# Optimization experiments

Measured on AMD Instinct MI355X. Metric: run time of the kernel, lower is better.

The kernel has to match this reference:

```python
import jax, jax.numpy as jnp
import numpy as np

E = 256   # embed_dim
H = 8     # num_heads
D = E // H  # head_dim = 32
L = 1024  # seq len (Q_len == K_len == V_len)


def setup_inputs() -> dict:
    key = jax.random.key(0)
    ks = jax.random.split(key, 10)
    f = lambda k, s: jax.random.normal(k, s, dtype=jnp.float32)
    return {
        "V": f(ks[0], (L, E)),
        "K": f(ks[1], (L, E)),
        "Q": f(ks[2], (L, E)),
        # genomic-style coordinates, strictly positive
        "position": jax.random.uniform(ks[3], (L,), dtype=jnp.float32) * 1e5,
        "Wq": f(ks[4], (E, E)) * 0.02,
        "Wk": f(ks[5], (E, E)) * 0.02,
        "Wv": f(ks[6], (E, E)) * 0.02,
        "Wr": f(ks[7], (E, 1)) * 0.02,   # K_relative_linear weight [out=E, in=1]
        "Wo": f(ks[8], (E, E)) * 0.02,
        "bo": jnp.zeros((E,), jnp.float32),
    }


def reference(V, K, Q, position, Wq, Wk, Wv, Wr, Wo, bo):
    Lq = Q.shape[0]
    # projections (nn.Linear: x @ W.T), split into heads -> (L, H, D)
    q = (Q @ Wq.T).reshape(Lq, H, D)
    k = (K @ Wk.T).reshape(Lq, H, D)
    v = (V @ Wv.T).reshape(Lq, H, D)

    # relative position scalar per (q, k) pair: log(|p_q - p_k| + 1)
    rel = jnp.log(jnp.abs(position[:, None] - position[None, :]) + 1.0)  # (L, L)

    # K_relative_linear maps scalar rel -> (H, D); the einsum
    # 'nqhd,nhqjd->nhqj' then factorizes exactly as:
    #   sum_d Q[q,h,d] * rel[q,j] * Wr[h,d] = (Q . Wr)[h,q] * rel[q,j]
    # so we avoid materializing the (H, L, L, D) tensor while computing
    # mathematically identical results.
    Wr_h = Wr[:, 0].reshape(H, D)                    # (H, D)
    coeff = jnp.einsum('qhd,hd->hq', q, Wr_h)        # (H, L)

    energy = jnp.einsum('qhd,khd->hqk', q, k)        # (H, L, L)
    energy = energy + coeff[:, :, None] * rel[None, :, :]

    attn = jax.nn.softmax(energy / np.float32(E) ** 0.5, axis=2)
    out = jnp.einsum('hqk,khd->qhd', attn, v).reshape(Lq, E)
    out = out @ Wo.T + bo
    return out
```

## Files before the change

### kernel.cpp

```cpp
#include <hip/hip_runtime.h>
#include <math.h>

#define EDIM 256
#define LDIM 1024
#define HDIM 8
#define DDIM 32

typedef __attribute__((ext_vector_type(8))) short short8;
typedef __attribute__((ext_vector_type(2))) short short2v;
typedef __attribute__((ext_vector_type(4))) short shortx4;
typedef __attribute__((ext_vector_type(4))) float f32x4;

__device__ inline unsigned short bf16h(float x) {
    unsigned u = __float_as_uint(x);
    return (unsigned short)((u + 0x7fff + ((u >> 16) & 1)) >> 16);
}
__device__ inline float bf16tof(unsigned short h) {
    return __uint_as_float(((unsigned)h) << 16);
}
__device__ inline float exp2fast(float x) {
    float r; asm volatile("v_exp_f32 %0, %1" : "=v"(r) : "v"(x)); return r;
}
__device__ inline float log2fast(float x) {
    float r; asm volatile("v_log_f32 %0, %1" : "=v"(r) : "v"(x)); return r;
}

#define SC2 0.09016843880556021f

__global__ __launch_bounds__(256) void proj_kernel(
    const float* __restrict__ Q, const float* __restrict__ Km, const float* __restrict__ V,
    const float* __restrict__ Wq, const float* __restrict__ Wk, const float* __restrict__ Wv,
    const float* __restrict__ Wr, const float* __restrict__ Wo,
    short* __restrict__ qThi, short* __restrict__ qTlo,
    short* __restrict__ kThi, short* __restrict__ kTlo,
    short* __restrict__ vThi, short* __restrict__ vTlo,
    float* __restrict__ coeff, short* __restrict__ Wohi, short* __restrict__ Wolo)
{
    const int z = blockIdx.z;
    const int tid = threadIdx.x;

    if (z == 3) {
        const int idx = ((blockIdx.y * 32 + blockIdx.x) << 8) + tid;
        const float w = Wo[idx];
        const unsigned short hh = bf16h(w);
        Wohi[idx] = (short)hh;
        Wolo[idx] = (short)bf16h(w - bf16tof(hh));
        return;
    }

    const float* __restrict__ X = (z == 0) ? Q : (z == 1) ? Km : V;
    const float* __restrict__ W = (z == 0) ? Wq : (z == 1) ? Wk : Wv;
    short* __restrict__ dhi     = (z == 0) ? qThi : (z == 1) ? kThi : vThi;
    short* __restrict__ dlo     = (z == 0) ? qTlo : (z == 1) ? kTlo : vTlo;

    const int n0 = blockIdx.x * 32;
    const int o0 = blockIdx.y * 32;
    const int wave = tid >> 6, lane = tid & 63;
    const int n = lane & 15, quad = lane >> 4;
    const int rh = wave & 1, oh = wave >> 1;

    const int s    = tid >> 7;
    const int r    = (tid >> 2) & 31;
    const int qd   = tid & 3;
    const int half = r >> 4;
    const int fl8  = ((r & 15) | (qd << 4)) * 8;

    __shared__ short Xhi[2][2][512], Xlo[2][2][512];
    __shared__ short Whi[2][2][512], Wlo[2][2][512];
    __shared__ float cpart[2][2][16];

    const float* xp = X + (n0 + r) * EDIM + s * 32 + qd * 8;
    const float* wp = W + (o0 + r) * EDIM + s * 32 + qd * 8;

    float4 xa0 = *(const float4*)xp, xa1 = *(const float4*)(xp + 4);
    float4 wa0 = *(const float4*)wp, wa1 = *(const float4*)(wp + 4);

    f32x4 acc = {0.f, 0.f, 0.f, 0.f};

    for (int kb = 0; kb < EDIM; kb += 64) {
        __syncthreads();
        {
            float xv[8] = {xa0.x,xa0.y,xa0.z,xa0.w, xa1.x,xa1.y,xa1.z,xa1.w};
            float wv[8] = {wa0.x,wa0.y,wa0.z,wa0.w, wa1.x,wa1.y,wa1.z,wa1.w};
            short8 xh, xl, wh, wl;
            #pragma unroll
            for (int j = 0; j < 8; ++j) {
                unsigned short xhh = bf16h(xv[j]);
                unsigned short whh = bf16h(wv[j]);
                xh[j] = (short)xhh; xl[j] = (short)bf16h(xv[j] - bf16tof(xhh));
                wh[j] = (short)whh; wl[j] = (short)bf16h(wv[j] - bf16tof(whh));
            }
            *(short8*)&Xhi[s][half][fl8] = xh;
            *(short8*)&Xlo[s][half][fl8] = xl;
            *(short8*)&Whi[s][half][fl8] = wh;
            *(short8*)&Wlo[s][half][fl8] = wl;
        }
        float4 xn0, xn1, wn0, wn1;
        if (kb + 64 < EDIM) {
            xn0 = *(const float4*)(xp + kb + 64); xn1 = *(const float4*)(xp + kb + 68);
            wn0 = *(const float4*)(wp + kb + 64); wn1 = *(const float4*)(wp + kb + 68);
        }
        __syncthreads();
        #pragma unroll
        for (int ss = 0; ss < 2; ++ss) {
            short8 ah = *(const short8*)&Xhi[ss][rh][lane*8];
            short8 al = *(const short8*)&Xlo[ss][rh][lane*8];
            short8 bh = *(const short8*)&Whi[ss][oh][lane*8];
            short8 bl = *(const short8*)&Wlo[ss][oh][lane*8];
            acc = __builtin_amdgcn_mfma_f32_16x16x32_bf16(al, bh, acc, 0, 0, 0);
            acc = __builtin_amdgcn_mfma_f32_16x16x32_bf16(ah, bl, acc, 0, 0, 0);
            acc = __builtin_amdgcn_mfma_f32_16x16x32_bf16(ah, bh, acc, 0, 0, 0);
        }
        xa0 = xn0; xa1 = xn1; wa0 = wn0; wa1 = wn1;
    }

    const int h  = o0 >> 5;
    const int og = oh * 16 + n;
    #pragma unroll
    for (int i = 0; i < 4; ++i) {
        const int row = rh * 16 + 4 * quad + i;
        const unsigned short hh = bf16h(acc[i]);
        dhi[(h * LDIM + n0 + row) * DDIM + og] = (short)hh;
        dlo[(h * LDIM + n0 + row) * DDIM + og] = (short)bf16h(acc[i] - bf16tof(hh));
    }

    if (z == 0) {
        const float wr = Wr[o0 + og];
        #pragma unroll
        for (int i = 0; i < 4; ++i) {
            float c = acc[i] * wr;
            c += __shfl_xor(c, 1, 64);
            c += __shfl_xor(c, 2, 64);
            c += __shfl_xor(c, 4, 64);
            c += __shfl_xor(c, 8, 64);
            if (n == 0) cpart[rh][oh][4*quad + i] = c;
        }
        __syncthreads();
        if (tid < 32)
            coeff[h * LDIM + n0 + tid] = cpart[tid >> 4][0][tid & 15]
                                       + cpart[tid >> 4][1][tid & 15];
    }
}

__global__ __launch_bounds__(256, 2) void attn_kernel(
    const short* __restrict__ qThi, const short* __restrict__ qTlo,
    const short* __restrict__ kThi, const short* __restrict__ kTlo,
    const short* __restrict__ vThi, const short* __restrict__ vTlo,
    const float* __restrict__ coeff, const float* __restrict__ pos,
    short* __restrict__ Ahi, short* __restrict__ Alo)
{
    const int h    = blockIdx.y;
    const int q0   = blockIdx.x * 16;
    const int tid  = threadIdx.x;
    const int wave = tid >> 6;
    const int lane = tid & 63;
    const int n    = lane & 15;
    const int quad = lane >> 4;

    __shared__ __align__(16) short vs_hi[4][32][72];
    __shared__ __align__(16) short vs_lo[4][32][72];
    __shared__ __align__(16) short pa_hi[4][16][72];
    __shared__ __align__(16) short pa_lo[4][16][72];
    __shared__ float mw[4][16], lw[4][16];
    __shared__ float Ow[4][16][36];

    const short8 qhi = *(const short8*)(qThi + (h*LDIM + q0 + n) * DDIM + quad*8);
    const short8 qlo = *(const short8*)(qTlo + (h*LDIM + q0 + n) * DDIM + quad*8);

    float pq[4], cq[4];
    #pragma unroll
    for (int i = 0; i < 4; ++i) {
        const int r = q0 + 4*quad + i;
        pq[i] = pos[r];
        cq[i] = coeff[h*LDIM + r] * 0.0625f;
    }

    float m[4], l[4];
    #pragma unroll
    for (int i = 0; i < 4; ++i) { m[i] = -INFINITY; l[i] = 0.f; }
    f32x4 of0 = {0.f,0.f,0.f,0.f}, of1 = {0.f,0.f,0.f,0.f};

    const int ktb = wave * 256;
    #pragma unroll 1
    for (int t = 0; t < 4; ++t) {
        const int kt = ktb + t * 64;

        {
            const short* vh = vThi + (h*LDIM + kt + lane) * DDIM;
            const short* vl = vTlo + (h*LDIM + kt + lane) * DDIM;
            #pragma unroll
            for (int hf = 0; hf < 2; ++hf) {
                short8 a0 = *(const short8*)(vh + hf*16);
                short8 a1 = *(const short8*)(vh + hf*16 + 8);
                short8 b0 = *(const short8*)(vl + hf*16);
                short8 b1 = *(const short8*)(vl + hf*16 + 8);
                #pragma unroll
                for (int j = 0; j < 8; ++j) {
                    vs_hi[wave][hf*16 + j][lane]     = a0[j];
                    vs_hi[wave][hf*16 + 8 + j][lane] = a1[j];
                    vs_lo[wave][hf*16 + j][lane]     = b0[j];
                    vs_lo[wave][hf*16 + 8 + j][lane] = b1[j];
                }
            }
        }

        f32x4 Sf[4];
        #pragma unroll
        for (int t4 = 0; t4 < 4; ++t4) {
            const int off = (h*LDIM + kt + t4*16 + n) * DDIM + quad*8;
            short8 bh = *(const short8*)(kThi + off);
            short8 bl = *(const short8*)(kTlo + off);
            f32x4 acc = {0.f, 0.f, 0.f, 0.f};
            acc = __builtin_amdgcn_mfma_f32_16x16x32_bf16(qlo, bh, acc, 0, 0, 0);
            acc = __builtin_amdgcn_mfma_f32_16x16x32_bf16(qhi, bl, acc, 0, 0, 0);
            acc = __builtin_amdgcn_mfma_f32_16x16x32_bf16(qhi, bh, acc, 0, 0, 0);
            Sf[t4] = acc;
        }

        float ev[4][4];
        float rmax[4] = {-INFINITY, -INFINITY, -INFINITY, -INFINITY};
        #pragma unroll
        for (int t4 = 0; t4 < 4; ++t4) {
            const float pkt = pos[kt + t4*16 + n];
            #pragma unroll
            for (int i = 0; i < 4; ++i) {
                float s = fmaf(Sf[t4][i], SC2, cq[i] * log2fast(fabsf(pq[i] - pkt) + 1.f));
                ev[t4][i] = s;
                rmax[i] = fmaxf(rmax[i], s);
            }
        }
        #pragma unroll
        for (int off = 1; off < 16; off <<= 1)
            #pragma unroll
            for (int i = 0; i < 4; ++i)
                rmax[i] = fmaxf(rmax[i], __shfl_xor(rmax[i], off, 64));

        float al[4], rsum[4];
        #pragma unroll
        for (int i = 0; i < 4; ++i) {
            const float mn = fmaxf(m[i], rmax[i]);
            al[i] = exp2fast(m[i] - mn);
            m[i] = mn;
            rsum[i] = 0.f;
        }
        #pragma unroll
        for (int t4 = 0; t4 < 4; ++t4)
            #pragma unroll
            for (int i = 0; i < 4; ++i) {
                float e = exp2fast(ev[t4][i] - m[i]);
                rsum[i] += e;
                unsigned u = __float_as_uint(e);
                pa_hi[wave][4*quad + i][16*t4 + n] = (short)(u >> 16);
                float r = e - __uint_as_float(u & 0xffff0000u);
                pa_lo[wave][4*quad + i][16*t4 + n] = (short)bf16h(r);
            }
        #pragma unroll
        for (int off = 1; off < 16; off <<= 1)
            #pragma unroll
            for (int i = 0; i < 4; ++i)
                rsum[i] += __shfl_xor(rsum[i], off, 64);
        #pragma unroll
        for (int i = 0; i < 4; ++i) l[i] = l[i]*al[i] + rsum[i];

        #pragma unroll
        for (int i = 0; i < 4; ++i) { of0[i] *= al[i]; of1[i] *= al[i]; }

        #pragma unroll
        for (int ch = 0; ch < 2; ++ch) {
            short8 phi = *(const short8*)&pa_hi[wave][n][ch*32 + quad*8];
            short8 plo = *(const short8*)&pa_lo[wave][n][ch*32 + quad*8];
            #pragma unroll
            for (int dt = 0; dt < 2; ++dt) {
                short8 vh8 = *(const short8*)&vs_hi[wave][dt*16 + n][ch*32 + quad*8];
                short8 vl8 = *(const short8*)&vs_lo[wave][dt*16 + n][ch*32 + quad*8];
                f32x4& of = dt ? of1 : of0;
                of = __builtin_amdgcn_mfma_f32_16x16x32_bf16(plo, vh8, of, 0, 0, 0);
                of = __builtin_amdgcn_mfma_f32_16x16x32_bf16(phi, vl8, of, 0, 0, 0);
                of = __builtin_amdgcn_mfma_f32_16x16x32_bf16(phi, vh8, of, 0, 0, 0);
            }
        }
    }

    #pragma unroll
    for (int i = 0; i < 4; ++i) {
        Ow[wave][4*quad + i][n]      = of0[i];
        Ow[wave][4*quad + i][16 + n] = of1[i];
    }
    if (n == 0) {
        #pragma unroll
        for (int i = 0; i < 4; ++i) {
            mw[wave][4*quad + i] = m[i];
            lw[wave][4*quad + i] = l[i];
        }
    }
    __syncthreads();

    {
        const int q  = tid >> 4;
        const int dp = (tid & 15) * 2;
        float M = fmaxf(fmaxf(mw[0][q], mw[1][q]), fmaxf(mw[2][q], mw[3][q]));
        float sc[4], s = 0.f;
        #pragma unroll
        for (int w = 0; w < 4; ++w) {
            sc[w] = exp2fast(mw[w][q] - M);
            s += sc[w] * lw[w][q];
        }
        const float inv = 1.f / s;
        short2v h2, l2;
        #pragma unroll
        for (int e = 0; e < 2; ++e) {
            float a = 0.f;
            #pragma unroll
            for (int w = 0; w < 4; ++w) a += sc[w] * Ow[w][q][dp + e];
            a *= inv;
            const unsigned short hh = bf16h(a);
            h2[e] = (short)hh;
            l2[e] = (short)bf16h(a - bf16tof(hh));
        }
        *(short2v*)(Ahi + (q0 + q)*EDIM + h*DDIM + dp) = h2;
        *(short2v*)(Alo + (q0 + q)*EDIM + h*DDIM + dp) = l2;
    }
}

__global__ __launch_bounds__(256) void outproj_kernel(
    const short* __restrict__ Ahi, const short* __restrict__ Alo,
    const short* __restrict__ Wohi, const short* __restrict__ Wolo,
    const float* __restrict__ bo, float* __restrict__ out)
{
    const int n0 = blockIdx.x * 32;
    const int o0 = blockIdx.y * 32;
    const int tid = threadIdx.x;
    const int wave = tid >> 6, lane = tid & 63;
    const int n = lane & 15, quad = lane >> 4;
    const int rh = wave & 1, oh = wave >> 1;

    const int s    = tid >> 7;
    const int r    = (tid >> 2) & 31;
    const int qd   = tid & 3;
    const int half = r >> 4;
    const int fl8  = ((r & 15) | (qd << 4)) * 8;

    __shared__ short Xhi[2][2][512], Xlo[2][2][512];
    __shared__ short Whi[2][2][512], Wlo[2][2][512];

    const short* xph = Ahi  + (n0 + r) * EDIM + s * 32 + qd * 8;
    const short* xpl = Alo  + (n0 + r) * EDIM + s * 32 + qd * 8;
    const short* wph = Wohi + (o0 + r) * EDIM + s * 32 + qd * 8;
    const short* wpl = Wolo + (o0 + r) * EDIM + s * 32 + qd * 8;

    short8 xh_c = *(const short8*)xph;
    short8 xl_c = *(const short8*)xpl;
    short8 wh_c = *(const short8*)wph;
    short8 wl_c = *(const short8*)wpl;

    f32x4 acc = {0.f, 0.f, 0.f, 0.f};

    for (int kb = 0; kb < EDIM; kb += 64) {
        __syncthreads();
        *(short8*)&Xhi[s][half][fl8] = xh_c;
        *(short8*)&Xlo[s][half][fl8] = xl_c;
        *(short8*)&Whi[s][half][fl8] = wh_c;
        *(short8*)&Wlo[s][half][fl8] = wl_c;
        short8 xh_n, xl_n, wh_n, wl_n;
        if (kb + 64 < EDIM) {
            xh_n = *(const short8*)(xph + kb + 64);
            xl_n = *(const short8*)(xpl + kb + 64);
            wh_n = *(const short8*)(wph + kb + 64);
            wl_n = *(const short8*)(wpl + kb + 64);
        }
        __syncthreads();
        #pragma unroll
        for (int ss = 0; ss < 2; ++ss) {
            short8 ah = *(const short8*)&Xhi[ss][rh][lane*8];
            short8 al = *(const short8*)&Xlo[ss][rh][lane*8];
            short8 bh = *(const short8*)&Whi[ss][oh][lane*8];
            short8 bl = *(const short8*)&Wlo[ss][oh][lane*8];
            acc = __builtin_amdgcn_mfma_f32_16x16x32_bf16(al, bh, acc, 0, 0, 0);
            acc = __builtin_amdgcn_mfma_f32_16x16x32_bf16(ah, bl, acc, 0, 0, 0);
            acc = __builtin_amdgcn_mfma_f32_16x16x32_bf16(ah, bh, acc, 0, 0, 0);
        }
        xh_c = xh_n; xl_c = xl_n; wh_c = wh_n; wl_c = wl_n;
    }

    const int og = o0 + oh*16 + n;
    const float b = bo[og];
    #pragma unroll
    for (int i = 0; i < 4; ++i) {
        const int row = n0 + rh*16 + 4*quad + i;
        out[row * EDIM + og] = acc[i] + b;
    }
}

extern "C" void kernel_launch(void* const* d_in, const int* in_sizes, int n_in,
                              void* d_out, int out_size, void* d_ws, size_t ws_size,
                              hipStream_t stream) {
    const float* V   = (const float*)d_in[0];
    const float* K   = (const float*)d_in[1];
    const float* Q   = (const float*)d_in[2];
    const float* pos = (const float*)d_in[3];
    const float* Wq  = (const float*)d_in[4];
    const float* Wk  = (const float*)d_in[5];
    const float* Wv  = (const float*)d_in[6];
    const float* Wr  = (const float*)d_in[7];
    const float* Wo  = (const float*)d_in[8];
    const float* bo  = (const float*)d_in[9];
    float* out = (float*)d_out;
    char* base = (char*)d_ws;

    short* qThi  = (short*)(base);
    short* qTlo  = (short*)(base + 524288);
    short* kThi  = (short*)(base + 1048576);
    short* kTlo  = (short*)(base + 1572864);
    short* vThi  = (short*)(base + 2097152);
    short* vTlo  = (short*)(base + 2621440);
    float* coeff = (float*)(base + 3145728);
    short* Wohi  = (short*)(base + 3178496);
    short* Wolo  = (short*)(base + 3309568);
    short* Ahi   = (short*)(base + 3440640);
    short* Alo   = (short*)(base + 3964928);

    proj_kernel   <<<dim3(32, 8, 4), 256, 0, stream>>>(Q, K, V, Wq, Wk, Wv, Wr, Wo,
                                                       qThi, qTlo, kThi, kTlo, vThi, vTlo,
                                                       coeff, Wohi, Wolo);
    attn_kernel   <<<dim3(64, 8),    256, 0, stream>>>(qThi, qTlo, kThi, kTlo, vThi, vTlo,
                                                       coeff, pos, Ahi, Alo);
    outproj_kernel<<<dim3(32, 8),    256, 0, stream>>>(Ahi, Alo, Wohi, Wolo, bo, out);
}
```

Baseline: 101.0 us.

## Fuse projection, attention and output projection into one persistent kernel with grid barriers

Replaces the three separate kernel launches with a single 512-block kernel. Each block performs two projection tiles, then one attention tile, then at most one output-projection tile, with atomic-counter grid barriers between the phases. Shared memory is a union of the two phase layouts. This removes launch overhead and inter-kernel gaps, but adds a memset and spin barriers, and correctness depends on all 512 blocks being co-resident.

```diff
diff --git a/kernel.cpp b/kernel.cpp
--- a/kernel.cpp
+++ b/kernel.cpp
@@ -8,7 +8,6 @@
 
 typedef __attribute__((ext_vector_type(8))) short short8;
 typedef __attribute__((ext_vector_type(2))) short short2v;
-typedef __attribute__((ext_vector_type(4))) short shortx4;
 typedef __attribute__((ext_vector_type(4))) float f32x4;
 
 __device__ inline unsigned short bf16h(float x) {
@@ -27,367 +26,390 @@
 
 #define SC2 0.09016843880556021f
 
-__global__ __launch_bounds__(256) void proj_kernel(
+#define NBLK 512
+
+__device__ inline void grid_barrier(unsigned* cnt) {
+    __syncthreads();
+    if (threadIdx.x == 0) {
+        __threadfence();
+        atomicAdd(cnt, 1u);
+        while (atomicAdd(cnt, 0u) < NBLK) __builtin_amdgcn_s_sleep(2);
+    }
+    __syncthreads();
+    __threadfence();
+}
+
+struct __align__(16) SmemProj {
+    short Xhi[2][2][512], Xlo[2][2][512];
+    short Whi[2][2][512], Wlo[2][2][512];
+    float cpart[2][2][16];
+};
+struct __align__(16) SmemAttn {
+    short vs_hi[4][32][72], vs_lo[4][32][72];
+    short pa_hi[4][16][72], pa_lo[4][16][72];
+    float mw[4][16], lw[4][16];
+    float Ow[4][16][36];
+};
+union SmemU {
+    SmemProj p;
+    SmemAttn a;
+};
+
+__global__ __launch_bounds__(256, 2) void mega_kernel(
     const float* __restrict__ Q, const float* __restrict__ Km, const float* __restrict__ V,
+    const float* __restrict__ pos,
     const float* __restrict__ Wq, const float* __restrict__ Wk, const float* __restrict__ Wv,
-    const float* __restrict__ Wr, const float* __restrict__ Wo,
-    short* __restrict__ qThi, short* __restrict__ qTlo,
-    short* __restrict__ kThi, short* __restrict__ kTlo,
-    short* __restrict__ vThi, short* __restrict__ vTlo,
-    float* __restrict__ coeff, short* __restrict__ Wohi, short* __restrict__ Wolo)
+    const float* __restrict__ Wr, const float* __restrict__ Wo, const float* __restrict__ bo,
+    float* __restrict__ out, char* __restrict__ base)
 {
-    const int z = blockIdx.z;
+    __shared__ SmemU sm;
+
+    short* qThi  = (short*)(base);
+    short* qTlo  = (short*)(base + 524288);
+    short* kThi  = (short*)(base + 1048576);
+    short* kTlo  = (short*)(base + 1572864);
+    short* vThi  = (short*)(base + 2097152);
+    short* vTlo  = (short*)(base + 2621440);
+    float* coeff = (float*)(base + 3145728);
+    short* Wohi  = (short*)(base + 3178496);
+    short* Wolo  = (short*)(base + 3309568);
+    short* Ahi   = (short*)(base + 3440640);
+    short* Alo   = (short*)(base + 3964928);
+    unsigned* flags = (unsigned*)(base + 4489216);
+
     const int tid = threadIdx.x;
-
-    if (z == 3) {
-        const int idx = ((blockIdx.y * 32 + blockIdx.x) << 8) + tid;
-        const float w = Wo[idx];
-        const unsigned short hh = bf16h(w);
-        Wohi[idx] = (short)hh;
-        Wolo[idx] = (short)bf16h(w - bf16tof(hh));
-        return;
-    }
-
-    const float* __restrict__ X = (z == 0) ? Q : (z == 1) ? Km : V;
-    const float* __restrict__ W = (z == 0) ? Wq : (z == 1) ? Wk : Wv;
-    short* __restrict__ dhi     = (z == 0) ? qThi : (z == 1) ? kThi : vThi;
-    short* __restrict__ dlo     = (z == 0) ? qTlo : (z == 1) ? kTlo : vTlo;
-
-    const int n0 = blockIdx.x * 32;
-    const int o0 = blockIdx.y * 32;
+    const int bid = blockIdx.x;
+
     const int wave = tid >> 6, lane = tid & 63;
     const int n = lane & 15, quad = lane >> 4;
-    const int rh = wave & 1, oh = wave >> 1;
-
-    const int s    = tid >> 7;
-    const int r    = (tid >> 2) & 31;
-    const int qd   = tid & 3;
-    const int half = r >> 4;
-    const int fl8  = ((r & 15) | (qd << 4)) * 8;
-
-    __shared__ short Xhi[2][2][512], Xlo[2][2][512];
-    __shared__ short Whi[2][2][512], Wlo[2][2][512];
-    __shared__ float cpart[2][2][16];
-
-    const float* xp = X + (n0 + r) * EDIM + s * 32 + qd * 8;
-    const float* wp = W + (o0 + r) * EDIM + s * 32 + qd * 8;
-
-    float4 xa0 = *(const float4*)xp, xa1 = *(const float4*)(xp + 4);
-    float4 wa0 = *(const float4*)wp, wa1 = *(const float4*)(wp + 4);
-
-    f32x4 acc = {0.f, 0.f, 0.f, 0.f};
-
-    for (int kb = 0; kb < EDIM; kb += 64) {
-        __syncthreads();
-        {
-            float xv[8] = {xa0.x,xa0.y,xa0.z,xa0.w, xa1.x,xa1.y,xa1.z,xa1.w};
-            float wv[8] = {wa0.x,wa0.y,wa0.z,wa0.w, wa1.x,wa1.y,wa1.z,wa1.w};
-            short8 xh, xl, wh, wl;
-            #pragma unroll
-            for (int j = 0; j < 8; ++j) {
-                unsigned short xhh = bf16h(xv[j]);
-                unsigned short whh = bf16h(wv[j]);
-                xh[j] = (short)xhh; xl[j] = (short)bf16h(xv[j] - bf16tof(xhh));
-                wh[j] = (short)whh; wl[j] = (short)bf16h(wv[j] - bf16tof(whh));
-            }
-            *(short8*)&Xhi[s][half][fl8] = xh;
-            *(short8*)&Xlo[s][half][fl8] = xl;
-            *(short8*)&Whi[s][half][fl8] = wh;
-            *(short8*)&Wlo[s][half][fl8] = wl;
-        }
-        float4 xn0, xn1, wn0, wn1;
-        if (kb + 64 < EDIM) {
-            xn0 = *(const float4*)(xp + kb + 64); xn1 = *(const float4*)(xp + kb + 68);
-            wn0 = *(const float4*)(wp + kb + 64); wn1 = *(const float4*)(wp + kb + 68);
-        }
-        __syncthreads();
-        #pragma unroll
-        for (int ss = 0; ss < 2; ++ss) {
-            short8 ah = *(const short8*)&Xhi[ss][rh][lane*8];
-            short8 al = *(const short8*)&Xlo[ss][rh][lane*8];
-            short8 bh = *(const short8*)&Whi[ss][oh][lane*8];
-            short8 bl = *(const short8*)&Wlo[ss][oh][lane*8];
-            acc = __builtin_amdgcn_mfma_f32_16x16x32_bf16(al, bh, acc, 0, 0, 0);
-            acc = __builtin_amdgcn_mfma_f32_16x16x32_bf16(ah, bl, acc, 0, 0, 0);
-            acc = __builtin_amdgcn_mfma_f32_16x16x32_bf16(ah, bh, acc, 0, 0, 0);
-        }
-        xa0 = xn0; xa1 = xn1; wa0 = wn0; wa1 = wn1;
+
+    {
+        const int rh = wave & 1, oh = wave >> 1;
+        const int s    = tid >> 7;
+        const int r    = (tid >> 2) & 31;
+        const int qd   = tid & 3;
+        const int half = r >> 4;
+        const int fl8  = ((r & 15) | (qd << 4)) * 8;
+
+        for (int ui = 0; ui < 2; ++ui) {
+            const int u = bid * 2 + ui;
+            const int z = u >> 8;
+            const int x = u & 31, y = (u >> 5) & 7;
+
+            if (z == 3) {
+                const int idx = ((y * 32 + x) << 8) + tid;
+                const float w = Wo[idx];
+                const unsigned short hh = bf16h(w);
+                Wohi[idx] = (short)hh;
+                Wolo[idx] = (short)bf16h(w - bf16tof(hh));
+                continue;
+            }
+
+            const float* __restrict__ X = (z == 0) ? Q : (z == 1) ? Km : V;
+            const float* __restrict__ W = (z == 0) ? Wq : (z == 1) ? Wk : Wv;
+            short* __restrict__ dhi     = (z == 0) ? qThi : (z == 1) ? kThi : vThi;
+            short* __restrict__ dlo     = (z == 0) ? qTlo : (z == 1) ? kTlo : vTlo;
+            const int n0 = x * 32;
+            const int o0 = y * 32;
+
+            const float* xp = X + (n0 + r) * EDIM + s * 32 + qd * 8;
+            const float* wp = W + (o0 + r) * EDIM + s * 32 + qd * 8;
+
+            float4 xa0 = *(const float4*)xp, xa1 = *(const float4*)(xp + 4);
+            float4 wa0 = *(const float4*)wp, wa1 = *(const float4*)(wp + 4);
+
+            f32x4 acc = {0.f, 0.f, 0.f, 0.f};
+
+            for (int kb = 0; kb < EDIM; kb += 64) {
+                __syncthreads();
+                {
+                    float xv[8] = {xa0.x,xa0.y,xa0.z,xa0.w, xa1.x,xa1.y,xa1.z,xa1.w};
+                    float wv[8] = {wa0.x,wa0.y,wa0.z,wa0.w, wa1.x,wa1.y,wa1.z,wa1.w};
+                    short8 xh, xl, wh, wl;
+                    #pragma unroll
+                    for (int j = 0; j < 8; ++j) {
+                        unsigned short xhh = bf16h(xv[j]);
+                        unsigned short whh = bf16h(wv[j]);
+                        xh[j] = (short)xhh; xl[j] = (short)bf16h(xv[j] - bf16tof(xhh));
+                        wh[j] = (short)whh; wl[j] = (short)bf16h(wv[j] - bf16tof(whh));
+                    }
+                    *(short8*)&sm.p.Xhi[s][half][fl8] = xh;
+                    *(short8*)&sm.p.Xlo[s][half][fl8] = xl;
+                    *(short8*)&sm.p.Whi[s][half][fl8] = wh;
+                    *(short8*)&sm.p.Wlo[s][half][fl8] = wl;
+                }
+                float4 xn0, xn1, wn0, wn1;
+                if (kb + 64 < EDIM) {
+                    xn0 = *(const float4*)(xp + kb + 64); xn1 = *(const float4*)(xp + kb + 68);
+                    wn0 = *(const float4*)(wp + kb + 64); wn1 = *(const float4*)(wp + kb + 68);
+                }
+                __syncthreads();
+                #pragma unroll
+                for (int ss = 0; ss < 2; ++ss) {
+                    short8 ah = *(const short8*)&sm.p.Xhi[ss][rh][lane*8];
+                    short8 al = *(const short8*)&sm.p.Xlo[ss][rh][lane*8];
+                    short8 bh = *(const short8*)&sm.p.Whi[ss][oh][lane*8];
+                    short8 bl = *(const short8*)&sm.p.Wlo[ss][oh][lane*8];
+                    acc = __builtin_amdgcn_mfma_f32_16x16x32_bf16(al, bh, acc, 0, 0, 0);
+                    acc = __builtin_amdgcn_mfma_f32_16x16x32_bf16(ah, bl, acc, 0, 0, 0);
+                    acc = __builtin_amdgcn_mfma_f32_16x16x32_bf16(ah, bh, acc, 0, 0, 0);
+                }
+                xa0 = xn0; xa1 = xn1; wa0 = wn0; wa1 = wn1;
+            }
+
+            const int h  = o0 >> 5;
+            const int og = oh * 16 + n;
+            #pragma unroll
+            for (int i = 0; i < 4; ++i) {
+                const int row = rh * 16 + 4 * quad + i;
+                const unsigned short hh = bf16h(acc[i]);
+                dhi[(h * LDIM + n0 + row) * DDIM + og] = (short)hh;
+                dlo[(h * LDIM + n0 + row) * DDIM + og] = (short)bf16h(acc[i] - bf16tof(hh));
+            }
+
+            if (z == 0) {
+                const float wr = Wr[o0 + og];
+                #pragma unroll
+                for (int i = 0; i < 4; ++i) {
+                    float c = acc[i] * wr;
+                    c += __shfl_xor(c, 1, 64);
+                    c += __shfl_xor(c, 2, 64);
+                    c += __shfl_xor(c, 4, 64);
+                    c += __shfl_xor(c, 8, 64);
+                    if (n == 0) sm.p.cpart[rh][oh][4*quad + i] = c;
+                }
+                __syncthreads();
+                if (tid < 32)
+                    coeff[h * LDIM + n0 + tid] = sm.p.cpart[tid >> 4][0][tid & 15]
+                                               + sm.p.cpart[tid >> 4][1][tid & 15];
+            }
+        }
     }
 
-    const int h  = o0 >> 5;
-    const int og = oh * 16 + n;
-    #pragma unroll
-    for (int i = 0; i < 4; ++i) {
-        const int row = rh * 16 + 4 * quad + i;
-        const unsigned short hh = bf16h(acc[i]);
-        dhi[(h * LDIM + n0 + row) * DDIM + og] = (short)hh;
-        dlo[(h * LDIM + n0 + row) * DDIM + og] = (short)bf16h(acc[i] - bf16tof(hh));
-    }
-
-    if (z == 0) {
-        const float wr = Wr[o0 + og];
+    grid_barrier(&flags[0]);
+
+    {
+        const int h  = bid >> 6;
+        const int q0 = (bid & 63) * 16;
+
+        const short8 qhi = *(const short8*)(qThi + (h*LDIM + q0 + n) * DDIM + quad*8);
+        const short8 qlo = *(const short8*)(qTlo + (h*LDIM + q0 + n) * DDIM + quad*8);
+
+        float pq[4], cq[4];
         #pragma unroll
         for (int i = 0; i < 4; ++i) {
-            float c = acc[i] * wr;
-            c += __shfl_xor(c, 1, 64);
-            c += __shfl_xor(c, 2, 64);
-            c += __shfl_xor(c, 4, 64);
-            c += __shfl_xor(c, 8, 64);
-            if (n == 0) cpart[rh][oh][4*quad + i] = c;
-        }
-        __syncthreads();
-        if (tid < 32)
-            coeff[h * LDIM + n0 + tid] = cpart[tid >> 4][0][tid & 15]
-                                       + cpart[tid >> 4][1][tid & 15];
-    }
-}
-
-__global__ __launch_bounds__(256, 2) void attn_kernel(
-    const short* __restrict__ qThi, const short* __restrict__ qTlo,
-    const short* __restrict__ kThi, const short* __restrict__ kTlo,
-    const short* __restrict__ vThi, const short* __restrict__ vTlo,
-    const float* __restrict__ coeff, const float* __restrict__ pos,
-    short* __restrict__ Ahi, short* __restrict__ Alo)
-{
-    const int h    = blockIdx.y;
-    const int q0   = blockIdx.x * 16;
-    const int tid  = threadIdx.x;
-    const int wave = tid >> 6;
-    const int lane = tid & 63;
-    const int n    = lane & 15;
-    const int quad = lane >> 4;
-
-    __shared__ __align__(16) short vs_hi[4][32][72];
-    __shared__ __align__(16) short vs_lo[4][32][72];
-    __shared__ __align__(16) short pa_hi[4][16][72];
-    __shared__ __align__(16) short pa_lo[4][16][72];
-    __shared__ float mw[4][16], lw[4][16];
-    __shared__ float Ow[4][16][36];
-
-    const short8 qhi = *(const short8*)(qThi + (h*LDIM + q0 + n) * DDIM + quad*8);
-    const short8 qlo = *(const short8*)(qTlo + (h*LDIM + q0 + n) * DDIM + quad*8);
-
-    float pq[4], cq[4];
-    #pragma unroll
-    for (int i = 0; i < 4; ++i) {
-        const int r = q0 + 4*quad + i;
-        pq[i] = pos[r];
-        cq[i] = coeff[h*LDIM + r] * 0.0625f;
-    }
-
-    float m[4], l[4];
-    #pragma unroll
-    for (int i = 0; i < 4; ++i) { m[i] = -INFINITY; l[i] = 0.f; }
-    f32x4 of0 = {0.f,0.f,0.f,0.f}, of1 = {0.f,0.f,0.f,0.f};
-
-    const int ktb = wave * 256;
-    #pragma unroll 1
-    for (int t = 0; t < 4; ++t) {
-        const int kt = ktb + t * 64;
-
-        {
-            const short* vh = vThi + (h*LDIM + kt + lane) * DDIM;
-            const short* vl = vTlo + (h*LDIM + kt + lane) * DDIM;
-            #pragma unroll
-            for (int hf = 0; hf < 2; ++hf) {
-                short8 a0 = *(const short8*)(vh + hf*16);
-                short8 a1 = *(const short8*)(vh + hf*16 + 8);
-                short8 b0 = *(const short8*)(vl + hf*16);
-                short8 b1 = *(const short8*)(vl + hf*16 + 8);
-                #pragma unroll
-                for (int j = 0; j < 8; ++j) {
-                    vs_hi[wave][hf*16 + j][lane]     = a0[j];
-                    vs_hi[wave][hf*16 + 8 + j][lane] = a1[j];
-                    vs_lo[wave][hf*16 + j][lane]     = b0[j];
-                    vs_lo[wave][hf*16 + 8 + j][lane] = b1[j];
-                }
-            }
-        }
-
-        f32x4 Sf[4];
+            const int r = q0 + 4*quad + i;
+            pq[i] = pos[r];
+            cq[i] = coeff[h*LDIM + r] * 0.0625f;
+        }
+
+        float m[4], l[4];
         #pragma unroll
-        for (int t4 = 0; t4 < 4; ++t4) {
-            const int off = (h*LDIM + kt + t4*16 + n) * DDIM + quad*8;
-            short8 bh = *(const short8*)(kThi + off);
-            short8 bl = *(const short8*)(kTlo + off);
-            f32x4 acc = {0.f, 0.f, 0.f, 0.f};
-            acc = __builtin_amdgcn_mfma_f32_16x16x32_bf16(qlo, bh, acc, 0, 0, 0);
-            acc = __builtin_amdgcn_mfma_f32_16x16x32_bf16(qhi, bl, acc, 0, 0, 0);
-            acc = __builtin_amdgcn_mfma_f32_16x16x32_bf16(qhi, bh, acc, 0, 0, 0);
-            Sf[t4] = acc;
-        }
-
-        float ev[4][4];
-        float rmax[4] = {-INFINITY, -INFINITY, -INFINITY, -INFINITY};
-        #pragma unroll
-        for (int t4 = 0; t4 < 4; ++t4) {
-            const float pkt = pos[kt + t4*16 + n];
+        for (int i = 0; i < 4; ++i) { m[i] = -INFINITY; l[i] = 0.f; }
+        f32x4 of0 = {0.f,0.f,0.f,0.f}, of1 = {0.f,0.f,0.f,0.f};
+
+        const int ktb = wave * 256;
+        #pragma unroll 1
+        for (int t = 0; t < 4; ++t) {
+            const int kt = ktb + t * 64;
+
+            {
+                const short* vh = vThi + (h*LDIM + kt + lane) * DDIM;
+                const short* vl = vTlo + (h*LDIM + kt + lane) * DDIM;
+                #pragma unroll
+                for (int hf = 0; hf < 2; ++hf) {
+                    short8 a0 = *(const short8*)(vh + hf*16);
+                    short8 a1 = *(const short8*)(vh + hf*16 + 8);
+                    short8 b0 = *(const short8*)(vl + hf*16);
+                    short8 b1 = *(const short8*)(vl + hf*16 + 8);
+                    #pragma unroll
+                    for (int j = 0; j < 8; ++j) {
+                        sm.a.vs_hi[wave][hf*16 + j][lane]     = a0[j];
+                        sm.a.vs_hi[wave][hf*16 + 8 + j][lane] = a1[j];
+                        sm.a.vs_lo[wave][hf*16 + j][lane]     = b0[j];
+                        sm.a.vs_lo[wave][hf*16 + 8 + j][lane] = b1[j];
+                    }
+                }
+            }
+
+            f32x4 Sf[4];
+            #pragma unroll
+            for (int t4 = 0; t4 < 4; ++t4) {
+                const int off = (h*LDIM + kt + t4*16 + n) * DDIM + quad*8;
+                short8 bh = *(const short8*)(kThi + off);
+                short8 bl = *(const short8*)(kTlo + off);
+                f32x4 acc = {0.f, 0.f, 0.f, 0.f};
+                acc = __builtin_amdgcn_mfma_f32_16x16x32_bf16(qlo, bh, acc, 0, 0, 0);
+                acc = __builtin_amdgcn_mfma_f32_16x16x32_bf16(qhi, bl, acc, 0, 0, 0);
+                acc = __builtin_amdgcn_mfma_f32_16x16x32_bf16(qhi, bh, acc, 0, 0, 0);
+                Sf[t4] = acc;
+            }
+
+            float ev[4][4];
+            float rmax[4] = {-INFINITY, -INFINITY, -INFINITY, -INFINITY};
+            #pragma unroll
+            for (int t4 = 0; t4 < 4; ++t4) {
+                const float pkt = pos[kt + t4*16 + n];
+                #pragma unroll
+                for (int i = 0; i < 4; ++i) {
+                    float s = fmaf(Sf[t4][i], SC2, cq[i] * log2fast(fabsf(pq[i] - pkt) + 1.f));
+                    ev[t4][i] = s;
+                    rmax[i] = fmaxf(rmax[i], s);
+                }
+            }
+            #pragma unroll
+            for (int off = 1; off < 16; off <<= 1)
+                #pragma unroll
+                for (int i = 0; i < 4; ++i)
+                    rmax[i] = fmaxf(rmax[i], __shfl_xor(rmax[i], off, 64));
+
+            float al[4], rsum[4];
             #pragma unroll
             for (int i = 0; i < 4; ++i) {
-                float s = fmaf(Sf[t4][i], SC2, cq[i] * log2fast(fabsf(pq[i] - pkt) + 1.f));
-                ev[t4][i] = s;
-                rmax[i] = fmaxf(rmax[i], s);
-            }
-        }
-        #pragma unroll
-        for (int off = 1; off < 16; off <<= 1)
-            #pragma unroll
-            for (int i = 0; i < 4; ++i)
-                rmax[i] = fmaxf(rmax[i], __shfl_xor(rmax[i], off, 64));
-
-        float al[4], rsum[4];
+                const float mn = fmaxf(m[i], rmax[i]);
+                al[i] = exp2fast(m[i] - mn);
+                m[i] = mn;
+                rsum[i] = 0.f;
+            }
+            #pragma unroll
+            for (int t4 = 0; t4 < 4; ++t4)
+                #pragma unroll
+                for (int i = 0; i < 4; ++i) {
+                    float e = exp2fast(ev[t4][i] - m[i]);
+                    rsum[i] += e;
+                    unsigned u = __float_as_uint(e);
+                    sm.a.pa_hi[wave][4*quad + i][16*t4 + n] = (short)(u >> 16);
+                    float r = e - __uint_as_float(u & 0xffff0000u);
+                    sm.a.pa_lo[wave][4*quad + i][16*t4 + n] = (short)bf16h(r);
+                }
+            #pragma unroll
+            for (int off = 1; off < 16; off <<= 1)
+                #pragma unroll
+                for (int i = 0; i < 4; ++i)
+                    rsum[i] += __shfl_xor(rsum[i], off, 64);
+            #pragma unroll
+            for (int i = 0; i < 4; ++i) l[i] = l[i]*al[i] + rsum[i];
+
+            #pragma unroll
+            for (int i = 0; i < 4; ++i) { of0[i] *= al[i]; of1[i] *= al[i]; }
+
+            #pragma unroll
+            for (int ch = 0; ch < 2; ++ch) {
+                short8 phi = *(const short8*)&sm.a.pa_hi[wave][n][ch*32 + quad*8];
+                short8 plo = *(const short8*)&sm.a.pa_lo[wave][n][ch*32 + quad*8];
+                #pragma unroll
+                for (int dt = 0; dt < 2; ++dt) {
+                    short8 vh8 = *(const short8*)&sm.a.vs_hi[wave][dt*16 + n][ch*32 + quad*8];
+                    short8 vl8 = *(const short8*)&sm.a.vs_lo[wave][dt*16 + n][ch*32 + quad*8];
+                    f32x4& of = dt ? of1 : of0;
+                    of = __builtin_amdgcn_mfma_f32_16x16x32_bf16(plo, vh8, of, 0, 0, 0);
+                    of = __builtin_amdgcn_mfma_f32_16x16x32_bf16(phi, vl8, of, 0, 0, 0);
+                    of = __builtin_amdgcn_mfma_f32_16x16x32_bf16(phi, vh8, of, 0, 0, 0);
+                }
+            }
+        }
+
         #pragma unroll
         for (int i = 0; i < 4; ++i) {
-            const float mn = fmaxf(m[i], rmax[i]);
-            al[i] = exp2fast(m[i] - mn);
-            m[i] = mn;
-            rsum[i] = 0.f;
-        }
-        #pragma unroll
-        for (int t4 = 0; t4 < 4; ++t4)
+            sm.a.Ow[wave][4*quad + i][n]      = of0[i];
+            sm.a.Ow[wave][4*quad + i][16 + n] = of1[i];
+        }
+        if (n == 0) {
             #pragma unroll
             for (int i = 0; i < 4; ++i) {
-                float e = exp2fast(ev[t4][i] - m[i]);
-                rsum[i] += e;
-                unsigned u = __float_as_uint(e);
-                pa_hi[wave][4*quad + i][16*t4 + n] = (short)(u >> 16);
-                float r = e - __uint_as_float(u & 0xffff0000u);
-                pa_lo[wave][4*quad + i][16*t4 + n] = (short)bf16h(r);
-            }
-        #pragma unroll
-        for (int off = 1; off < 16; off <<= 1)
-            #pragma unroll
-            for (int i = 0; i < 4; ++i)
-                rsum[i] += __shfl_xor(rsum[i], off, 64);
-        #pragma unroll
-        for (int i = 0; i < 4; ++i) l[i] = l[i]*al[i] + rsum[i];
-
-        #pragma unroll
-        for (int i = 0; i < 4; ++i) { of0[i] *= al[i]; of1[i] *= al[i]; }
-
-        #pragma unroll
-        for (int ch = 0; ch < 2; ++ch) {
-            short8 phi = *(const short8*)&pa_hi[wave][n][ch*32 + quad*8];
-            short8 plo = *(const short8*)&pa_lo[wave][n][ch*32 + quad*8];
-            #pragma unroll
-            for (int dt = 0; dt < 2; ++dt) {
-                short8 vh8 = *(const short8*)&vs_hi[wave][dt*16 + n][ch*32 + quad*8];
-                short8 vl8 = *(const short8*)&vs_lo[wave][dt*16 + n][ch*32 + quad*8];
-                f32x4& of = dt ? of1 : of0;
-                of = __builtin_amdgcn_mfma_f32_16x16x32_bf16(plo, vh8, of, 0, 0, 0);
-                of = __builtin_amdgcn_mfma_f32_16x16x32_bf16(phi, vl8, of, 0, 0, 0);
-                of = __builtin_amdgcn_mfma_f32_16x16x32_bf16(phi, vh8, of, 0, 0, 0);
-            }
+                sm.a.mw[wave][4*quad + i] = m[i];
+                sm.a.lw[wave][4*quad + i] = l[i];
+            }
+        }
+        __syncthreads();
+
+        {
+            const int q  = tid >> 4;
+            const int dp = (tid & 15) * 2;
+            float M = fmaxf(fmaxf(sm.a.mw[0][q], sm.a.mw[1][q]),
+                            fmaxf(sm.a.mw[2][q], sm.a.mw[3][q]));
+            float sc[4], s = 0.f;
+            #pragma unroll
+            for (int w = 0; w < 4; ++w) {
+                sc[w] = exp2fast(sm.a.mw[w][q] - M);
+                s += sc[w] * sm.a.lw[w][q];
+            }
+            const float inv = 1.f / s;
+            short2v h2, l2;
+            #pragma unroll
+            for (int e = 0; e < 2; ++e) {
+                float a = 0.f;
+                #pragma unroll
+                for (int w = 0; w < 4; ++w) a += sc[w] * sm.a.Ow[w][q][dp + e];
+                a *= inv;
+                const unsigned short hh = bf16h(a);
+                h2[e] = (short)hh;
+                l2[e] = (short)bf16h(a - bf16tof(hh));
+            }
+            *(short2v*)(Ahi + (q0 + q)*EDIM + h*DDIM + dp) = h2;
+            *(short2v*)(Alo + (q0 + q)*EDIM + h*DDIM + dp) = l2;
         }
     }
 
-    #pragma unroll
-    for (int i = 0; i < 4; ++i) {
-        Ow[wave][4*quad + i][n]      = of0[i];
-        Ow[wave][4*quad + i][16 + n] = of1[i];
-    }
-    if (n == 0) {
+    grid_barrier(&flags[1]);
+
+    if (bid < 256) {
+        const int n0 = (bid & 31) * 32;
+        const int o0 = (bid >> 5) * 32;
+        const int rh = wave & 1, oh = wave >> 1;
+
+        const int s    = tid >> 7;
+        const int r    = (tid >> 2) & 31;
+        const int qd   = tid & 3;
+        const int half = r >> 4;
+        const int fl8  = ((r & 15) | (qd << 4)) * 8;
+
+        const short* xph = Ahi  + (n0 + r) * EDIM + s * 32 + qd * 8;
+        const short* xpl = Alo  + (n0 + r) * EDIM + s * 32 + qd * 8;
+        const short* wph = Wohi + (o0 + r) * EDIM + s * 32 + qd * 8;
+        const short* wpl = Wolo + (o0 + r) * EDIM + s * 32 + qd * 8;
+
+        short8 xh_c = *(const short8*)xph;
+        short8 xl_c = *(const short8*)xpl;
+        short8 wh_c = *(const short8*)wph;
+        short8 wl_c = *(const short8*)wpl;
+
+        f32x4 acc = {0.f, 0.f, 0.f, 0.f};
+
+        for (int kb = 0; kb < EDIM; kb += 64) {
+            __syncthreads();
+            *(short8*)&sm.p.Xhi[s][half][fl8] = xh_c;
+            *(short8*)&sm.p.Xlo[s][half][fl8] = xl_c;
+            *(short8*)&sm.p.Whi[s][half][fl8] = wh_c;
+            *(short8*)&sm.p.Wlo[s][half][fl8] = wl_c;
+            short8 xh_n, xl_n, wh_n, wl_n;
+            if (kb + 64 < EDIM) {
+                xh_n = *(const short8*)(xph + kb + 64);
+                xl_n = *(const short8*)(xpl + kb + 64);
+                wh_n = *(const short8*)(wph + kb + 64);
+                wl_n = *(const short8*)(wpl + kb + 64);
+            }
+            __syncthreads();
+            #pragma unroll
+            for (int ss = 0; ss < 2; ++ss) {
+                short8 ah = *(const short8*)&sm.p.Xhi[ss][rh][lane*8];
+                short8 al = *(const short8*)&sm.p.Xlo[ss][rh][lane*8];
+                short8 bh = *(const short8*)&sm.p.Whi[ss][oh][lane*8];
+                short8 bl = *(const short8*)&sm.p.Wlo[ss][oh][lane*8];
+                acc = __builtin_amdgcn_mfma_f32_16x16x32_bf16(al, bh, acc, 0, 0, 0);
+                acc = __builtin_amdgcn_mfma_f32_16x16x32_bf16(ah, bl, acc, 0, 0, 0);
+                acc = __builtin_amdgcn_mfma_f32_16x16x32_bf16(ah, bh, acc, 0, 0, 0);
+            }
+            xh_c = xh_n; xl_c = xl_n; wh_c = wh_n; wl_c = wl_n;
+        }
+
+        const int og = o0 + oh*16 + n;
+        const float b = bo[og];
         #pragma unroll
         for (int i = 0; i < 4; ++i) {
-            mw[wave][4*quad + i] = m[i];
-            lw[wave][4*quad + i] = l[i];
-        }
-    }
-    __syncthreads();
-
-    {
-        const int q  = tid >> 4;
-        const int dp = (tid & 15) * 2;
-        float M = fmaxf(fmaxf(mw[0][q], mw[1][q]), fmaxf(mw[2][q], mw[3][q]));
-        float sc[4], s = 0.f;
-        #pragma unroll
-        for (int w = 0; w < 4; ++w) {
-            sc[w] = exp2fast(mw[w][q] - M);
-            s += sc[w] * lw[w][q];
-        }
-        const float inv = 1.f / s;
-        short2v h2, l2;
-        #pragma unroll
-        for (int e = 0; e < 2; ++e) {
-            float a = 0.f;
-            #pragma unroll
-            for (int w = 0; w < 4; ++w) a += sc[w] * Ow[w][q][dp + e];
-            a *= inv;
-            const unsigned short hh = bf16h(a);
-            h2[e] = (short)hh;
-            l2[e] = (short)bf16h(a - bf16tof(hh));
-        }
-        *(short2v*)(Ahi + (q0 + q)*EDIM + h*DDIM + dp) = h2;
-        *(short2v*)(Alo + (q0 + q)*EDIM + h*DDIM + dp) = l2;
-    }
-}
-
-__global__ __launch_bounds__(256) void outproj_kernel(
-    const short* __restrict__ Ahi, const short* __restrict__ Alo,
-    const short* __restrict__ Wohi, const short* __restrict__ Wolo,
-    const float* __restrict__ bo, float* __restrict__ out)
-{
-    const int n0 = blockIdx.x * 32;
-    const int o0 = blockIdx.y * 32;
-    const int tid = threadIdx.x;
-    const int wave = tid >> 6, lane = tid & 63;
-    const int n = lane & 15, quad = lane >> 4;
-    const int rh = wave & 1, oh = wave >> 1;
-
-    const int s    = tid >> 7;
-    const int r    = (tid >> 2) & 31;
-    const int qd   = tid & 3;
-    const int half = r >> 4;
-    const int fl8  = ((r & 15) | (qd << 4)) * 8;
-
-    __shared__ short Xhi[2][2][512], Xlo[2][2][512];
-    __shared__ short Whi[2][2][512], Wlo[2][2][512];
-
-    const short* xph = Ahi  + (n0 + r) * EDIM + s * 32 + qd * 8;
-    const short* xpl = Alo  + (n0 + r) * EDIM + s * 32 + qd * 8;
-    const short* wph = Wohi + (o0 + r) * EDIM + s * 32 + qd * 8;
-    const short* wpl = Wolo + (o0 + r) * EDIM + s * 32 + qd * 8;
-
-    short8 xh_c = *(const short8*)xph;
-    short8 xl_c = *(const short8*)xpl;
-    short8 wh_c = *(const short8*)wph;
-    short8 wl_c = *(const short8*)wpl;
-
-    f32x4 acc = {0.f, 0.f, 0.f, 0.f};
-
-    for (int kb = 0; kb < EDIM; kb += 64) {
-        __syncthreads();
-        *(short8*)&Xhi[s][half][fl8] = xh_c;
-        *(short8*)&Xlo[s][half][fl8] = xl_c;
-        *(short8*)&Whi[s][half][fl8] = wh_c;
-        *(short8*)&Wlo[s][half][fl8] = wl_c;
-        short8 xh_n, xl_n, wh_n, wl_n;
-        if (kb + 64 < EDIM) {
-            xh_n = *(const short8*)(xph + kb + 64);
-            xl_n = *(const short8*)(xpl + kb + 64);
-            wh_n = *(const short8*)(wph + kb + 64);
-            wl_n = *(const short8*)(wpl + kb + 64);
-        }
-        __syncthreads();
-        #pragma unroll
-        for (int ss = 0; ss < 2; ++ss) {
-            short8 ah = *(const short8*)&Xhi[ss][rh][lane*8];
-            short8 al = *(const short8*)&Xlo[ss][rh][lane*8];
-            short8 bh = *(const short8*)&Whi[ss][oh][lane*8];
-            short8 bl = *(const short8*)&Wlo[ss][oh][lane*8];
-            acc = __builtin_amdgcn_mfma_f32_16x16x32_bf16(al, bh, acc, 0, 0, 0);
-            acc = __builtin_amdgcn_mfma_f32_16x16x32_bf16(ah, bl, acc, 0, 0, 0);
-            acc = __builtin_amdgcn_mfma_f32_16x16x32_bf16(ah, bh, acc, 0, 0, 0);
-        }
-        xh_c = xh_n; xl_c = xl_n; wh_c = wh_n; wl_c = wl_n;
-    }
-
-    const int og = o0 + oh*16 + n;
-    const float b = bo[og];
-    #pragma unroll
-    for (int i = 0; i < 4; ++i) {
-        const int row = n0 + rh*16 + 4*quad + i;
-        out[row * EDIM + og] = acc[i] + b;
+            const int row = n0 + rh*16 + 4*quad + i;
+            out[row * EDIM + og] = acc[i] + b;
+        }
     }
 }
 
@@ -407,22 +429,7 @@
     float* out = (float*)d_out;
     char* base = (char*)d_ws;
 
-    short* qThi  = (short*)(base);
-    short* qTlo  = (short*)(base + 524288);
-    short* kThi  = (short*)(base + 1048576);
-    short* kTlo  = (short*)(base + 1572864);
-    short* vThi  = (short*)(base + 2097152);
-    short* vTlo  = (short*)(base + 2621440);
-    float* coeff = (float*)(base + 3145728);
-    short* Wohi  = (short*)(base + 3178496);
-    short* Wolo  = (short*)(base + 3309568);
-    short* Ahi   = (short*)(base + 3440640);
-    short* Alo   = (short*)(base + 3964928);
-
-    proj_kernel   <<<dim3(32, 8, 4), 256, 0, stream>>>(Q, K, V, Wq, Wk, Wv, Wr, Wo,
-                                                       qThi, qTlo, kThi, kTlo, vThi, vTlo,
-                                                       coeff, Wohi, Wolo);
-    attn_kernel   <<<dim3(64, 8),    256, 0, stream>>>(qThi, qTlo, kThi, kTlo, vThi, vTlo,
-                                                       coeff, pos, Ahi, Alo);
-    outproj_kernel<<<dim3(32, 8),    256, 0, stream>>>(Ahi, Alo, Wohi, Wolo, bo, out);
-}
+    hipMemsetAsync(base + 4489216, 0, 64, stream);
+    mega_kernel<<<dim3(NBLK), dim3(256), 0, stream>>>(
+        Q, K, V, pos, Wq, Wk, Wv, Wr, Wo, bo, out, base);
+}
```

New measurement: 232.4 us. +130.1%, slower.
